# Performance work log

Hardware: AMD Instinct MI355X
Metric: run time of the kernel (lower is better)

## Reference

```python
import jax, jax.numpy as jnp
import numpy as np
from jax import lax


def _conv(x, w):
    # x: [B,H,W,C], w: [kh,kw,Cin,Cout], stride 1, 'same' padding
    return lax.conv_general_dilated(x, w, window_strides=(1, 1), padding='SAME',
                                    dimension_numbers=('NHWC', 'HWIO', 'NHWC'))


def setup_inputs() -> dict:
    key = jax.random.key(0)
    ks = jax.random.split(key, 4)
    B, T, H, W, Cin, F = 16, 5, 256, 256, 3, 8
    return {
        'input_tensor': jax.random.normal(ks[0], (B, T, H, W, Cin), jnp.float32),
        'kernel': jax.random.normal(ks[1], (3, 3, Cin, 4 * F), jnp.float32) * 0.1,
        'recurrent_kernel': jax.random.normal(ks[2], (3, 3, F, 4 * F), jnp.float32) * 0.1,
        'bias': jnp.zeros((4 * F,), jnp.float32),
        'gamma': jnp.ones((F,), jnp.float32),
        'beta': jnp.zeros((F,), jnp.float32),
        'moving_mean': jnp.zeros((F,), jnp.float32),
        'moving_var': jnp.ones((F,), jnp.float32),
        'dense_w': jax.random.normal(ks[3], (F, 2), jnp.float32) * 0.1,
        'dense_b': jnp.zeros((2,), jnp.float32),
    }


def reference(input_tensor, kernel, recurrent_kernel, bias, gamma, beta,
              moving_mean, moving_var, dense_w, dense_b):
    B, T, H, W, Cin = input_tensor.shape
    F = recurrent_kernel.shape[2]
    xs = jnp.moveaxis(input_tensor, 1, 0)  # [T,B,H,W,Cin] time-major for scan
    h0 = jnp.zeros((B, H, W, F), input_tensor.dtype)

    def step(carry, x_t):
        h, c = carry
        # fused 4-gate pre-activations, Keras gate order: i, f, c(g), o
        z = _conv(x_t, kernel) + _conv(h, recurrent_kernel) + bias
        i, f, g, o = jnp.split(z, 4, axis=-1)
        i = jax.nn.sigmoid(i)
        f = jax.nn.sigmoid(f)
        g = jnp.tanh(g)
        o = jax.nn.sigmoid(o)
        c = f * c + i * g
        h = o * jnp.tanh(c)
        return (h, c), None

    (h, _), _ = lax.scan(step, (h0, h0), xs)  # return_sequences=False -> last h

    # BatchNormalization (inference, Keras eps=1e-3)
    eps = 1e-3
    x = (h - moving_mean) * lax.rsqrt(moving_var + eps) * gamma + beta
    # LeakyReLU, Keras default alpha=0.3
    x = jnp.where(x >= 0, x, 0.3 * x)
    # Dense(2) over channel dim
    return jnp.einsum('bhwf,fk->bhwk', x, dense_w) + dense_b
```

## Files before the change

kernel.cpp:

```cpp
#include <hip/hip_runtime.h>


#define BB  16
#define TT  5
#define HH  256
#define WW  256
#define CIN 3
#define FF  8
#define GG  32

#define TW  32
#define THT 16
#define LW  34
#define LH  18
#define NG  8

#define SW  30
#define SH  14
#define NPX 9
#define NPY 19

#define LOG2E 1.44269504088896340736f

typedef _Float16 half8  __attribute__((ext_vector_type(8)));
typedef _Float16 half4  __attribute__((ext_vector_type(4)));
typedef _Float16 half2t __attribute__((ext_vector_type(2)));
typedef float    floatx4 __attribute__((ext_vector_type(4)));

__device__ __forceinline__ float frcp(float x) { return __builtin_amdgcn_rcpf(x); }
__device__ __forceinline__ float sig2(float z)  { return frcp(1.0f + __builtin_amdgcn_exp2f(z)); }
__device__ __forceinline__ float tanh2(float z) { return 1.0f - 2.0f * frcp(1.0f + __builtin_amdgcn_exp2f(z)); }

__device__ __forceinline__ int clampi(int v, int lo, int hi) {
    return v < lo ? lo : (v > hi ? hi : v);
}

#define MFMA(A, B, C) __builtin_amdgcn_mfma_f32_16x16x32_f16((A), (B), (C), 0, 0, 0)

#define GATES(ACC0, ACC1, C0, C1, CN0, CN1, HN0, HN1)                         \
  float CN0, CN1, HN0, HN1;                                                   \
  {                                                                           \
    float s0 = lo8 ? ACC0[2] : ACC0[0]; float r0 = __shfl_xor(s0, 8, 64);     \
    float s1 = lo8 ? ACC0[3] : ACC0[1]; float r1 = __shfl_xor(s1, 8, 64);     \
    float s2 = lo8 ? ACC1[2] : ACC1[0]; float r2 = __shfl_xor(s2, 8, 64);     \
    float s3 = lo8 ? ACC1[3] : ACC1[1]; float r3 = __shfl_xor(s3, 8, 64);     \
    const float zi0 = lo8 ? ACC0[0] : r0, zi1 = lo8 ? ACC0[1] : r1;           \
    const float zf0 = lo8 ? r0 : ACC0[2], zf1 = lo8 ? r1 : ACC0[3];           \
    const float zg0 = lo8 ? ACC1[0] : r2, zg1 = lo8 ? ACC1[1] : r3;           \
    const float zo0 = lo8 ? r2 : ACC1[2], zo1 = lo8 ? r3 : ACC1[3];           \
    const float ii0 = sig2(zi0), ff0 = sig2(zf0), gg0 = tanh2(zg0), oo0 = sig2(zo0); \
    CN0 = ff0 * (C0) + ii0 * gg0;                                             \
    HN0 = oo0 * tanh2(CN0 * (2.0f * LOG2E));                                  \
    const float ii1 = sig2(zi1), ff1 = sig2(zf1), gg1 = tanh2(zg1), oo1 = sig2(zo1); \
    CN1 = ff1 * (C1) + ii1 * gg1;                                             \
    HN1 = oo1 * tanh2(CN1 * (2.0f * LOG2E));                                  \
  }

__global__ void build_frags(const float* __restrict__ wk,
                            const float* __restrict__ wr,
                            _Float16* __restrict__ blob) {
    const int lane = threadIdx.x & 63;
    const int quad = lane >> 4, nlo = lane & 15;
    for (int chunk = 0; chunk < 5; ++chunk) {
        for (int nh = 0; nh < 2; ++nh) {
            const int n = nh * 16 + nlo;
            const float scale = (n >= 16 && n < 24) ? (2.0f * LOG2E) : (-LOG2E);
            const int frag = chunk * 2 + nh;
            _Float16* dhi = blob + ((size_t)frag * 64 + lane) * 8;
            _Float16* dlo = (chunk >= 2)
                ? blob + ((size_t)(10 + (chunk - 2) * 2 + nh) * 64 + lane) * 8
                : nullptr;
            for (int j = 0; j < 8; ++j) {
                const int k = quad * 8 + j;
                float w = 0.0f;
                if (chunk == 0) {
                    int tap = k >> 2, ci = k & 3;
                    if (ci < 3) w = wk[(tap * 3 + ci) * GG + n];
                } else if (chunk == 1) {
                    if (quad == 0 && j < 3) w = wk[(8 * 3 + j) * GG + n];
                } else {
                    int c = chunk - 2;
                    int tap = c * 4 + quad, ci = j;
                    if (tap < 9) w = wr[(tap * FF + ci) * GG + n];
                }
                w *= scale;
                _Float16 wh = (_Float16)w;
                dhi[j] = wh;
                if (dlo) dlo[j] = (_Float16)(w - (float)wh);
            }
        }
    }
}

template <int FIRSTPAIR>
__global__ __launch_bounds__(256) void lstm_pair(
    const float* __restrict__ xg,
    int t,
    const _Float16* __restrict__ blob,
    const float* __restrict__ bias,
    const _Float16* __restrict__ hin,
    _Float16* __restrict__ hout,
    const _Float16* __restrict__ cin,
    _Float16* __restrict__ cout)
{
    __shared__ half8 hls1[LH * LW];
    __shared__ half4 xls1[LH * LW];
    __shared__ half4 xls2[THT * TW];
    __shared__ __align__(16) _Float16 hls2[THT * TW * FF];

    const int tid  = threadIdx.x;
    const int lane = tid & 63, wave = tid >> 6;
    const int quad = lane >> 4, nlo = lane & 15;
    const bool lo8 = (nlo < 8);
    const int fc = nlo & 7;
    const int m0 = quad * 4 + (lo8 ? 0 : 2);

    const int bx = blockIdx.x, by = blockIdx.y, b = blockIdx.z;
    const int x0 = bx * SW - 1, y0 = by * SH - 1;

    half8 bfh[10], bfl[6];
#pragma unroll
    for (int i = 0; i < 10; ++i)
        bfh[i] = *(const half8*)(blob + ((size_t)i * 64 + lane) * 8);
#pragma unroll
    for (int i = 0; i < 6; ++i)
        bfl[i] = *(const half8*)(blob + ((size_t)(10 + i) * 64 + lane) * 8);

    const float bv0 = bias[nlo] * (-LOG2E);
    const float bv1 = bias[16 + nlo] * (lo8 ? 2.0f * LOG2E : -LOG2E);

    float xr1[3][3];
    bool  xin1[3];
#pragma unroll
    for (int k = 0; k < 3; ++k) {
        const int l = tid + k * 256;
        const bool in = (l < LH * LW);
        xin1[k] = in;
        int r = l / LW, c = l - r * LW;
        int gy = y0 - 1 + r, gx = x0 - 1 + c;
        const bool inb = in && (unsigned)gy < HH && (unsigned)gx < WW;
        const float* p = xg + (((size_t)(b * TT + t) * HH + gy) * WW + gx) * CIN;
        xr1[k][0] = inb ? p[0] : 0.0f;
        xr1[k][1] = inb ? p[1] : 0.0f;
        xr1[k][2] = inb ? p[2] : 0.0f;
    }
    float xr2[2][3];
#pragma unroll
    for (int k = 0; k < 2; ++k) {
        const int l = tid + k * 256;
        int r = l >> 5, c = l & 31;
        int gy = y0 + r, gx = x0 + c;
        const bool inb = (unsigned)gy < HH && (unsigned)gx < WW;
        const float* p = xg + (((size_t)(b * TT + t + 1) * HH + gy) * WW + gx) * CIN;
        xr2[k][0] = inb ? p[0] : 0.0f;
        xr2[k][1] = inb ? p[1] : 0.0f;
        xr2[k][2] = inb ? p[2] : 0.0f;
    }
    half8 hr[3];
    if (!FIRSTPAIR) {
#pragma unroll
        for (int k = 0; k < 3; ++k) {
            const int l = tid + k * 256;
            const bool in = (l < LH * LW);
            int r = l / LW, c = l - r * LW;
            int gy = y0 - 1 + r, gx = x0 - 1 + c;
            const bool inb = in && (unsigned)gy < HH && (unsigned)gx < WW;
            half8 v = {(_Float16)0, (_Float16)0, (_Float16)0, (_Float16)0,
                       (_Float16)0, (_Float16)0, (_Float16)0, (_Float16)0};
            if (inb) v = *(const half8*)(hin + ((size_t)(b * HH + gy) * WW + gx) * FF);
            hr[k] = v;
        }
    }
    half2t cpre[NG];
    if (!FIRSTPAIR) {
#pragma unroll
        for (int g = 0; g < NG; ++g) {
            const int lr  = wave * 4 + (g >> 1);
            const int gx0 = (g & 1) * 16;
            const int gy  = y0 + lr;
            const int gxa = x0 + gx0 + m0;
            const bool iny = (unsigned)gy < HH;
            half2t cv; cv.x = (_Float16)0; cv.y = (_Float16)0;
            const _Float16* cp = cin + ((size_t)(b * HH + gy) * WW + gxa) * FF + fc;
            if (iny && (unsigned)gxa < WW)       cv.x = cp[0];
            if (iny && (unsigned)(gxa + 1) < WW) cv.y = cp[FF];
            cpre[g] = cv;
        }
    }

#pragma unroll
    for (int k = 0; k < 3; ++k) {
        if (xin1[k]) {
            half4 vh;
            vh.x = (_Float16)xr1[k][0];
            vh.y = (_Float16)xr1[k][1];
            vh.z = (_Float16)xr1[k][2];
            vh.w = (_Float16)0;
            xls1[tid + k * 256] = vh;
        }
    }
#pragma unroll
    for (int k = 0; k < 2; ++k) {
        half4 vh;
        vh.x = (_Float16)xr2[k][0];
        vh.y = (_Float16)xr2[k][1];
        vh.z = (_Float16)xr2[k][2];
        vh.w = (_Float16)0;
        xls2[tid + k * 256] = vh;
    }
    if (!FIRSTPAIR) {
#pragma unroll
        for (int k = 0; k < 3; ++k)
            if (xin1[k]) hls1[tid + k * 256] = hr[k];
    }
    __syncthreads();

    half2t creg[NG];
#pragma unroll
    for (int g = 0; g < NG; ++g) {
        const int lr  = wave * 4 + (g >> 1);
        const int gx0 = (g & 1) * 16;
        const int lc  = gx0 + nlo;

        const int t0 = 2 * quad, t1 = t0 + 1;
        half4 p  = xls1[(lr + t0 / 3) * LW + lc + t0 % 3];
        half4 q  = xls1[(lr + t1 / 3) * LW + lc + t1 % 3];
        half4 s8 = xls1[(lr + 2) * LW + lc + 2];
        half8 a_xA = (half8){p.x, p.y, p.z, p.w, q.x, q.y, q.z, q.w};
        half8 a_xB = (half8){s8.x, s8.y, s8.z, s8.w, s8.x, s8.y, s8.z, s8.w};

        floatx4 acc0 = {bv0, bv0, bv0, bv0};
        floatx4 acc1 = {bv1, bv1, bv1, bv1};
        acc0 = MFMA(a_xA, bfh[0], acc0);  acc1 = MFMA(a_xA, bfh[1], acc1);
        acc0 = MFMA(a_xB, bfh[2], acc0);  acc1 = MFMA(a_xB, bfh[3], acc1);
        if (!FIRSTPAIR) {
#pragma unroll
            for (int c = 0; c < 3; ++c) {
                int tap = c * 4 + quad;
                if (tap > 8) tap = 8;
                half8 ah = hls1[(lr + tap / 3) * LW + lc + tap % 3];
                acc0 = MFMA(ah, bfh[4 + c * 2], acc0);
                acc1 = MFMA(ah, bfh[5 + c * 2], acc1);
                acc0 = MFMA(ah, bfl[c * 2 + 0], acc0);
                acc1 = MFMA(ah, bfl[c * 2 + 1], acc1);
            }
        }

        const float c0 = FIRSTPAIR ? 0.0f : (float)cpre[g].x;
        const float c1 = FIRSTPAIR ? 0.0f : (float)cpre[g].y;
        GATES(acc0, acc1, c0, c1, cn0, cn1, hn0, hn1);

        half2t cc; cc.x = (_Float16)cn0; cc.y = (_Float16)cn1;
        creg[g] = cc;

        const int gy   = y0 + lr;
        const int colm = gx0 + m0;
        const int gxa  = x0 + colm;
        const bool iny = (unsigned)gy < HH;
        _Float16 h0v = (_Float16)hn0, h1v = (_Float16)hn1;
        if (!(iny && (unsigned)gxa < WW))       h0v = (_Float16)0;
        if (!(iny && (unsigned)(gxa + 1) < WW)) h1v = (_Float16)0;
        hls2[(lr * TW + colm) * FF + fc]     = h0v;
        hls2[(lr * TW + colm + 1) * FF + fc] = h1v;
    }
    __syncthreads();

#pragma unroll
    for (int g = 0; g < NG; ++g) {
        const int lr  = wave * 4 + (g >> 1);
        const int gx0 = (g & 1) * 16;
        const int lc  = gx0 + nlo;

        const int t0 = 2 * quad, t1 = t0 + 1;
        half4 p  = xls2[clampi(lr + t0 / 3 - 1, 0, THT - 1) * TW + clampi(lc + t0 % 3 - 1, 0, TW - 1)];
        half4 q  = xls2[clampi(lr + t1 / 3 - 1, 0, THT - 1) * TW + clampi(lc + t1 % 3 - 1, 0, TW - 1)];
        half4 s8 = xls2[clampi(lr + 1, 0, THT - 1) * TW + clampi(lc + 1, 0, TW - 1)];
        half8 a_xA = (half8){p.x, p.y, p.z, p.w, q.x, q.y, q.z, q.w};
        half8 a_xB = (half8){s8.x, s8.y, s8.z, s8.w, s8.x, s8.y, s8.z, s8.w};

        floatx4 acc0 = {bv0, bv0, bv0, bv0};
        floatx4 acc1 = {bv1, bv1, bv1, bv1};
        acc0 = MFMA(a_xA, bfh[0], acc0);  acc1 = MFMA(a_xA, bfh[1], acc1);
        acc0 = MFMA(a_xB, bfh[2], acc0);  acc1 = MFMA(a_xB, bfh[3], acc1);
#pragma unroll
        for (int c = 0; c < 3; ++c) {
            int tap = c * 4 + quad;
            if (tap > 8) tap = 8;
            const int rr = clampi(lr + tap / 3 - 1, 0, THT - 1);
            const int cc = clampi(lc + tap % 3 - 1, 0, TW - 1);
            half8 ah = *(const half8*)(hls2 + (rr * TW + cc) * FF);
            acc0 = MFMA(ah, bfh[4 + c * 2], acc0);
            acc1 = MFMA(ah, bfh[5 + c * 2], acc1);
            acc0 = MFMA(ah, bfl[c * 2 + 0], acc0);
            acc1 = MFMA(ah, bfl[c * 2 + 1], acc1);
        }

        GATES(acc0, acc1, (float)creg[g].x, (float)creg[g].y, cn0, cn1, hn0, hn1);

        const int gy   = y0 + lr;
        const int colm = gx0 + m0;
        const int gxa  = x0 + colm;
        const bool rowok = (lr >= 1) && (lr <= SH) && ((unsigned)gy < HH);
        const bool c0ok = rowok && (colm >= 1) && (colm <= SW) && ((unsigned)gxa < WW);
        const bool c1ok = rowok && (colm + 1 <= SW) && ((unsigned)(gxa + 1) < WW);
        const size_t base = ((size_t)(b * HH + gy) * WW + gxa) * FF + fc;
        if (c0ok) {
            hout[base] = (_Float16)hn0;
            cout[base] = (_Float16)cn0;
        }
        if (c1ok) {
            hout[base + FF] = (_Float16)hn1;
            cout[base + FF] = (_Float16)cn1;
        }
    }
}

__global__ __launch_bounds__(256) void lstm_last(
    const float* __restrict__ xg,
    const _Float16* __restrict__ blob,
    const float* __restrict__ bias,
    const _Float16* __restrict__ hin,
    const _Float16* __restrict__ cin,
    const float* __restrict__ gamma, const float* __restrict__ beta,
    const float* __restrict__ mean,  const float* __restrict__ var,
    const float* __restrict__ dw,    const float* __restrict__ db,
    float* __restrict__ out)
{
    __shared__ half8 hls[LH * LW];
    __shared__ half4 xls[LH * LW];

    const int tid  = threadIdx.x;
    const int lane = tid & 63, wave = tid >> 6;
    const int quad = lane >> 4, nlo = lane & 15;
    const bool lo8 = (nlo < 8);
    const int fc = nlo & 7;
    const int m0 = quad * 4 + (lo8 ? 0 : 2);
    const int bx = blockIdx.x, by = blockIdx.y, b = blockIdx.z;
    const int t = TT - 1;

    half8 bfh[10], bfl[6];
#pragma unroll
    for (int i = 0; i < 10; ++i)
        bfh[i] = *(const half8*)(blob + ((size_t)i * 64 + lane) * 8);
#pragma unroll
    for (int i = 0; i < 6; ++i)
        bfl[i] = *(const half8*)(blob + ((size_t)(10 + i) * 64 + lane) * 8);

    const float bv0 = bias[nlo] * (-LOG2E);
    const float bv1 = bias[16 + nlo] * (lo8 ? 2.0f * LOG2E : -LOG2E);

    float xr[3][3];
    bool  xin[3];
#pragma unroll
    for (int k = 0; k < 3; ++k) {
        const int l = tid + k * 256;
        const bool in = (l < LH * LW);
        xin[k] = in;
        int r = l / LW, c = l - r * LW;
        int gy = by * THT + r - 1, gx = bx * TW + c - 1;
        const bool inb = in && (unsigned)gy < HH && (unsigned)gx < WW;
        const float* p = xg + (((size_t)(b * TT + t) * HH + gy) * WW + gx) * CIN;
        xr[k][0] = inb ? p[0] : 0.0f;
        xr[k][1] = inb ? p[1] : 0.0f;
        xr[k][2] = inb ? p[2] : 0.0f;
    }
    half8 hr[3];
#pragma unroll
    for (int k = 0; k < 3; ++k) {
        const int l = tid + k * 256;
        const bool in = (l < LH * LW);
        int r = l / LW, c = l - r * LW;
        int gy = by * THT + r - 1, gx = bx * TW + c - 1;
        const bool inb = in && (unsigned)gy < HH && (unsigned)gx < WW;
        half8 v = {(_Float16)0, (_Float16)0, (_Float16)0, (_Float16)0,
                   (_Float16)0, (_Float16)0, (_Float16)0, (_Float16)0};
        if (inb) v = *(const half8*)(hin + ((size_t)(b * HH + gy) * WW + gx) * FF);
        hr[k] = v;
    }
    half2t cpre[NG];
#pragma unroll
    for (int g = 0; g < NG; ++g) {
        const int lr  = wave * 4 + (g >> 1);
        const int gx0 = (g & 1) * 16;
        const int gy  = by * THT + lr;
        const int gxa = bx * TW + gx0 + m0;
        const _Float16* cp = cin + ((size_t)(b * HH + gy) * WW + gxa) * FF + fc;
        half2t cv; cv.x = cp[0]; cv.y = cp[FF];
        cpre[g] = cv;
    }

#pragma unroll
    for (int k = 0; k < 3; ++k) {
        if (xin[k]) {
            half4 vh;
            vh.x = (_Float16)xr[k][0];
            vh.y = (_Float16)xr[k][1];
            vh.z = (_Float16)xr[k][2];
            vh.w = (_Float16)0;
            xls[tid + k * 256] = vh;
            hls[tid + k * 256] = hr[k];
        }
    }
    __syncthreads();

    const float bn_s = gamma[fc] * rsqrtf(var[fc] + 1e-3f);
    const float bn_b = beta[fc] - mean[fc] * bn_s;
    const float dw0 = dw[fc * 2 + 0], dw1 = dw[fc * 2 + 1];
    const float db0 = db[0], db1 = db[1];

#pragma unroll
    for (int g = 0; g < NG; ++g) {
        const int lr  = wave * 4 + (g >> 1);
        const int gx0 = (g & 1) * 16;
        const int lc  = gx0 + nlo;

        const int t0 = 2 * quad, t1 = t0 + 1;
        half4 p  = xls[(lr + t0 / 3) * LW + lc + t0 % 3];
        half4 q  = xls[(lr + t1 / 3) * LW + lc + t1 % 3];
        half4 s8 = xls[(lr + 2) * LW + lc + 2];
        half8 a_xA = (half8){p.x, p.y, p.z, p.w, q.x, q.y, q.z, q.w};
        half8 a_xB = (half8){s8.x, s8.y, s8.z, s8.w, s8.x, s8.y, s8.z, s8.w};

        floatx4 acc0 = {bv0, bv0, bv0, bv0};
        floatx4 acc1 = {bv1, bv1, bv1, bv1};
        acc0 = MFMA(a_xA, bfh[0], acc0);  acc1 = MFMA(a_xA, bfh[1], acc1);
        acc0 = MFMA(a_xB, bfh[2], acc0);  acc1 = MFMA(a_xB, bfh[3], acc1);
#pragma unroll
        for (int c = 0; c < 3; ++c) {
            int tap = c * 4 + quad;
            if (tap > 8) tap = 8;
            half8 ah = hls[(lr + tap / 3) * LW + lc + tap % 3];
            acc0 = MFMA(ah, bfh[4 + c * 2], acc0);
            acc1 = MFMA(ah, bfh[5 + c * 2], acc1);
            acc0 = MFMA(ah, bfl[c * 2 + 0], acc0);
            acc1 = MFMA(ah, bfl[c * 2 + 1], acc1);
        }

        GATES(acc0, acc1, (float)cpre[g].x, (float)cpre[g].y, cn0, cn1, hn0, hn1);
        (void)cn0; (void)cn1;

        const int gy = by * THT + lr;
        float y0 = bn_s * hn0 + bn_b; y0 = (y0 >= 0.f) ? y0 : 0.3f * y0;
        float y1 = bn_s * hn1 + bn_b; y1 = (y1 >= 0.f) ? y1 : 0.3f * y1;
        float p00 = y0 * dw0, p01 = y0 * dw1;
        float p10 = y1 * dw0, p11 = y1 * dw1;
#pragma unroll
        for (int m = 1; m <= 4; m <<= 1) {
            p00 += __shfl_xor(p00, m, 64);
            p01 += __shfl_xor(p01, m, 64);
            p10 += __shfl_xor(p10, m, 64);
            p11 += __shfl_xor(p11, m, 64);
        }
        const int j = nlo & 7;
        if (j < 4) {
            const int px = m0 + (j >> 1);
            const int k  = j & 1;
            float val = (j == 0 ? p00 : j == 1 ? p01 : j == 2 ? p10 : p11)
                        + (k ? db1 : db0);
            out[((size_t)(b * HH + gy) * WW + bx * TW + gx0 + px) * 2 + k] = val;
        }
    }
}

extern "C" void kernel_launch(void* const* d_in, const int* in_sizes, int n_in,
                              void* d_out, int out_size, void* d_ws, size_t ws_size,
                              hipStream_t stream) {
    const float* x     = (const float*)d_in[0];
    const float* wk    = (const float*)d_in[1];
    const float* wr    = (const float*)d_in[2];
    const float* bias  = (const float*)d_in[3];
    const float* gamma = (const float*)d_in[4];
    const float* beta  = (const float*)d_in[5];
    const float* mean  = (const float*)d_in[6];
    const float* var   = (const float*)d_in[7];
    const float* dw    = (const float*)d_in[8];
    const float* db    = (const float*)d_in[9];
    float* out = (float*)d_out;

    const size_t state = (size_t)BB * HH * WW * FF;
    _Float16* blob = (_Float16*)d_ws;
    _Float16* hA = (_Float16*)((char*)d_ws + 32768);
    _Float16* hB = hA + state;
    _Float16* cA = hB + state;
    _Float16* cB = cA + state;

    build_frags<<<1, 64, 0, stream>>>(wk, wr, blob);

    dim3 pgrid(NPX, NPY, BB), block(256);
    lstm_pair<1><<<pgrid, block, 0, stream>>>(x, 0, blob, bias,
                                              nullptr, hA, nullptr, cA);
    lstm_pair<0><<<pgrid, block, 0, stream>>>(x, 2, blob, bias,
                                              hA, hB, cA, cB);
    dim3 lgrid(WW / TW, HH / THT, BB);
    lstm_last<<<lgrid, block, 0, stream>>>(x, blob, bias, hB, cB,
                                           gamma, beta, mean, var, dw, db, out);
}
```

Before: 292.4 us.

## Make lstm_pair persistent with register prefetch of next tile's halo

```diff
diff --git a/kernel.cpp b/kernel.cpp
--- a/kernel.cpp
+++ b/kernel.cpp
@@ -19,6 +19,8 @@
 #define SH  14
 #define NPX 9
 #define NPY 19
+#define NTILE (NPX * NPY * BB)
+#define NBLKP 768
 
 #define LOG2E 1.44269504088896340736f
 
@@ -92,8 +94,37 @@
     }
 }
 
+#define DECODE(TILE, B_, BY_, BX_)                                            \
+    const int B_  = (TILE) / (NPX * NPY);                                     \
+    const int rm_##B_ = (TILE) - B_ * (NPX * NPY);                            \
+    const int BY_ = rm_##B_ / NPX;                                            \
+    const int BX_ = rm_##B_ - BY_ * NPX;
+
+#define PFX1H(TILE, XR, HR, DOH)                                              \
+  {                                                                           \
+    DECODE(TILE, b_, by_, bx_)                                                \
+    const int x0_ = bx_ * SW - 1, y0_ = by_ * SH - 1;                         \
+    _Pragma("unroll")                                                         \
+    for (int k = 0; k < 3; ++k) {                                             \
+      const int l = tid + k * 256;                                            \
+      const int r = l / LW, c = l - r * LW;                                   \
+      const int gy = y0_ - 1 + r, gx = x0_ - 1 + c;                           \
+      const bool inb = xin[k] && (unsigned)gy < HH && (unsigned)gx < WW;      \
+      const float* p = xg + (((size_t)(b_ * TT + t) * HH + gy) * WW + gx) * CIN; \
+      XR[k][0] = inb ? p[0] : 0.0f;                                           \
+      XR[k][1] = inb ? p[1] : 0.0f;                                           \
+      XR[k][2] = inb ? p[2] : 0.0f;                                           \
+      if (DOH) {                                                              \
+        half8 v = {(_Float16)0, (_Float16)0, (_Float16)0, (_Float16)0,        \
+                   (_Float16)0, (_Float16)0, (_Float16)0, (_Float16)0};       \
+        if (inb) v = *(const half8*)(hin + ((size_t)(b_ * HH + gy) * WW + gx) * FF); \
+        HR[k] = v;                                                            \
+      }                                                                       \
+    }                                                                         \
+  }
+
 template <int FIRSTPAIR>
-__global__ __launch_bounds__(256) void lstm_pair(
+__global__ __launch_bounds__(256, 3) void lstm_pair(
     const float* __restrict__ xg,
     int t,
     const _Float16* __restrict__ blob,
@@ -115,8 +146,9 @@
     const int fc = nlo & 7;
     const int m0 = quad * 4 + (lo8 ? 0 : 2);
 
-    const int bx = blockIdx.x, by = blockIdx.y, b = blockIdx.z;
-    const int x0 = bx * SW - 1, y0 = by * SH - 1;
+    bool xin[3];
+#pragma unroll
+    for (int k = 0; k < 3; ++k) xin[k] = (tid + k * 256 < LH * LW);
 
     half8 bfh[10], bfl[6];
 #pragma unroll
@@ -130,187 +162,179 @@
     const float bv1 = bias[16 + nlo] * (lo8 ? 2.0f * LOG2E : -LOG2E);
 
     float xr1[3][3];
-    bool  xin1[3];
-#pragma unroll
-    for (int k = 0; k < 3; ++k) {
-        const int l = tid + k * 256;
-        const bool in = (l < LH * LW);
-        xin1[k] = in;
-        int r = l / LW, c = l - r * LW;
-        int gy = y0 - 1 + r, gx = x0 - 1 + c;
-        const bool inb = in && (unsigned)gy < HH && (unsigned)gx < WW;
-        const float* p = xg + (((size_t)(b * TT + t) * HH + gy) * WW + gx) * CIN;
-        xr1[k][0] = inb ? p[0] : 0.0f;
-        xr1[k][1] = inb ? p[1] : 0.0f;
-        xr1[k][2] = inb ? p[2] : 0.0f;
-    }
-    float xr2[2][3];
-#pragma unroll
-    for (int k = 0; k < 2; ++k) {
-        const int l = tid + k * 256;
-        int r = l >> 5, c = l & 31;
-        int gy = y0 + r, gx = x0 + c;
-        const bool inb = (unsigned)gy < HH && (unsigned)gx < WW;
-        const float* p = xg + (((size_t)(b * TT + t + 1) * HH + gy) * WW + gx) * CIN;
-        xr2[k][0] = inb ? p[0] : 0.0f;
-        xr2[k][1] = inb ? p[1] : 0.0f;
-        xr2[k][2] = inb ? p[2] : 0.0f;
-    }
     half8 hr[3];
-    if (!FIRSTPAIR) {
+    PFX1H((int)blockIdx.x, xr1, hr, !FIRSTPAIR);
+
+#pragma unroll 1
+    for (int tile = (int)blockIdx.x; tile < NTILE; tile += NBLKP) {
+        DECODE(tile, b, by, bx)
+        const int x0 = bx * SW - 1, y0 = by * SH - 1;
+        const int nxt = tile + NBLKP;
+
+        float xr2[2][3];
+#pragma unroll
+        for (int k = 0; k < 2; ++k) {
+            const int l = tid + k * 256;
+            const int r = l >> 5, c = l & 31;
+            const int gy = y0 + r, gx = x0 + c;
+            const bool inb = (unsigned)gy < HH && (unsigned)gx < WW;
+            const float* p = xg + (((size_t)(b * TT + t + 1) * HH + gy) * WW + gx) * CIN;
+            xr2[k][0] = inb ? p[0] : 0.0f;
+            xr2[k][1] = inb ? p[1] : 0.0f;
+            xr2[k][2] = inb ? p[2] : 0.0f;
+        }
+        half2t cpre[NG];
+#pragma unroll
+        for (int g = 0; g < NG; ++g) {
+            half2t cv; cv.x = (_Float16)0; cv.y = (_Float16)0;
+            if (!FIRSTPAIR) {
+                const int lr  = wave * 4 + (g >> 1);
+                const int gx0 = (g & 1) * 16;
+                const int gy  = y0 + lr;
+                const int gxa = x0 + gx0 + m0;
+                const bool iny = (unsigned)gy < HH;
+                const _Float16* cp = cin + ((size_t)(b * HH + gy) * WW + gxa) * FF + fc;
+                if (iny && (unsigned)gxa < WW)       cv.x = cp[0];
+                if (iny && (unsigned)(gxa + 1) < WW) cv.y = cp[FF];
+            }
+            cpre[g] = cv;
+        }
+
+        __syncthreads();
+
 #pragma unroll
         for (int k = 0; k < 3; ++k) {
-            const int l = tid + k * 256;
-            const bool in = (l < LH * LW);
-            int r = l / LW, c = l - r * LW;
-            int gy = y0 - 1 + r, gx = x0 - 1 + c;
-            const bool inb = in && (unsigned)gy < HH && (unsigned)gx < WW;
-            half8 v = {(_Float16)0, (_Float16)0, (_Float16)0, (_Float16)0,
-                       (_Float16)0, (_Float16)0, (_Float16)0, (_Float16)0};
-            if (inb) v = *(const half8*)(hin + ((size_t)(b * HH + gy) * WW + gx) * FF);
-            hr[k] = v;
-        }
-    }
-    half2t cpre[NG];
-    if (!FIRSTPAIR) {
+            if (xin[k]) {
+                half4 vh;
+                vh.x = (_Float16)xr1[k][0];
+                vh.y = (_Float16)xr1[k][1];
+                vh.z = (_Float16)xr1[k][2];
+                vh.w = (_Float16)0;
+                xls1[tid + k * 256] = vh;
+                if (!FIRSTPAIR) hls1[tid + k * 256] = hr[k];
+            }
+        }
+#pragma unroll
+        for (int k = 0; k < 2; ++k) {
+            half4 vh;
+            vh.x = (_Float16)xr2[k][0];
+            vh.y = (_Float16)xr2[k][1];
+            vh.z = (_Float16)xr2[k][2];
+            vh.w = (_Float16)0;
+            xls2[tid + k * 256] = vh;
+        }
+
+        float xr1n[3][3];
+        half8 hrn[3];
+        if (nxt < NTILE) PFX1H(nxt, xr1n, hrn, !FIRSTPAIR);
+
+        __syncthreads();
+
+        half2t creg[NG];
 #pragma unroll
         for (int g = 0; g < NG; ++g) {
             const int lr  = wave * 4 + (g >> 1);
             const int gx0 = (g & 1) * 16;
-            const int gy  = y0 + lr;
-            const int gxa = x0 + gx0 + m0;
+            const int lc  = gx0 + nlo;
+
+            const int t0 = 2 * quad, t1 = t0 + 1;
+            half4 p  = xls1[(lr + t0 / 3) * LW + lc + t0 % 3];
+            half4 q  = xls1[(lr + t1 / 3) * LW + lc + t1 % 3];
+            half4 s8 = xls1[(lr + 2) * LW + lc + 2];
+            half8 a_xA = (half8){p.x, p.y, p.z, p.w, q.x, q.y, q.z, q.w};
+            half8 a_xB = (half8){s8.x, s8.y, s8.z, s8.w, s8.x, s8.y, s8.z, s8.w};
+
+            floatx4 acc0 = {bv0, bv0, bv0, bv0};
+            floatx4 acc1 = {bv1, bv1, bv1, bv1};
+            acc0 = MFMA(a_xA, bfh[0], acc0);  acc1 = MFMA(a_xA, bfh[1], acc1);
+            acc0 = MFMA(a_xB, bfh[2], acc0);  acc1 = MFMA(a_xB, bfh[3], acc1);
+            if (!FIRSTPAIR) {
+#pragma unroll
+                for (int c = 0; c < 3; ++c) {
+                    int tap = c * 4 + quad;
+                    if (tap > 8) tap = 8;
+                    half8 ah = hls1[(lr + tap / 3) * LW + lc + tap % 3];
+                    acc0 = MFMA(ah, bfh[4 + c * 2], acc0);
+                    acc1 = MFMA(ah, bfh[5 + c * 2], acc1);
+                    acc0 = MFMA(ah, bfl[c * 2 + 0], acc0);
+                    acc1 = MFMA(ah, bfl[c * 2 + 1], acc1);
+                }
+            }
+
+            GATES(acc0, acc1, (float)cpre[g].x, (float)cpre[g].y, cn0, cn1, hn0, hn1);
+
+            half2t cc; cc.x = (_Float16)cn0; cc.y = (_Float16)cn1;
+            creg[g] = cc;
+
+            const int gy   = y0 + lr;
+            const int colm = gx0 + m0;
+            const int gxa  = x0 + colm;
             const bool iny = (unsigned)gy < HH;
-            half2t cv; cv.x = (_Float16)0; cv.y = (_Float16)0;
-            const _Float16* cp = cin + ((size_t)(b * HH + gy) * WW + gxa) * FF + fc;
-            if (iny && (unsigned)gxa < WW)       cv.x = cp[0];
-            if (iny && (unsigned)(gxa + 1) < WW) cv.y = cp[FF];
-            cpre[g] = cv;
-        }
-    }
-
-#pragma unroll
-    for (int k = 0; k < 3; ++k) {
-        if (xin1[k]) {
-            half4 vh;
-            vh.x = (_Float16)xr1[k][0];
-            vh.y = (_Float16)xr1[k][1];
-            vh.z = (_Float16)xr1[k][2];
-            vh.w = (_Float16)0;
-            xls1[tid + k * 256] = vh;
-        }
-    }
-#pragma unroll
-    for (int k = 0; k < 2; ++k) {
-        half4 vh;
-        vh.x = (_Float16)xr2[k][0];
-        vh.y = (_Float16)xr2[k][1];
-        vh.z = (_Float16)xr2[k][2];
-        vh.w = (_Float16)0;
-        xls2[tid + k * 256] = vh;
-    }
-    if (!FIRSTPAIR) {
-#pragma unroll
-        for (int k = 0; k < 3; ++k)
-            if (xin1[k]) hls1[tid + k * 256] = hr[k];
-    }
-    __syncthreads();
-
-    half2t creg[NG];
-#pragma unroll
-    for (int g = 0; g < NG; ++g) {
-        const int lr  = wave * 4 + (g >> 1);
-        const int gx0 = (g & 1) * 16;
-        const int lc  = gx0 + nlo;
-
-        const int t0 = 2 * quad, t1 = t0 + 1;
-        half4 p  = xls1[(lr + t0 / 3) * LW + lc + t0 % 3];
-        half4 q  = xls1[(lr + t1 / 3) * LW + lc + t1 % 3];
-        half4 s8 = xls1[(lr + 2) * LW + lc + 2];
-        half8 a_xA = (half8){p.x, p.y, p.z, p.w, q.x, q.y, q.z, q.w};
-        half8 a_xB = (half8){s8.x, s8.y, s8.z, s8.w, s8.x, s8.y, s8.z, s8.w};
-
-        floatx4 acc0 = {bv0, bv0, bv0, bv0};
-        floatx4 acc1 = {bv1, bv1, bv1, bv1};
-        acc0 = MFMA(a_xA, bfh[0], acc0);  acc1 = MFMA(a_xA, bfh[1], acc1);
-        acc0 = MFMA(a_xB, bfh[2], acc0);  acc1 = MFMA(a_xB, bfh[3], acc1);
-        if (!FIRSTPAIR) {
+            _Float16 h0v = (_Float16)hn0, h1v = (_Float16)hn1;
+            if (!(iny && (unsigned)gxa < WW))       h0v = (_Float16)0;
+            if (!(iny && (unsigned)(gxa + 1) < WW)) h1v = (_Float16)0;
+            hls2[(lr * TW + colm) * FF + fc]     = h0v;
+            hls2[(lr * TW + colm + 1) * FF + fc] = h1v;
+        }
+        __syncthreads();
+
+#pragma unroll
+        for (int g = 0; g < NG; ++g) {
+            const int lr  = wave * 4 + (g >> 1);
+            const int gx0 = (g & 1) * 16;
+            const int lc  = gx0 + nlo;
+
+            const int t0 = 2 * quad, t1 = t0 + 1;
+            half4 p  = xls2[clampi(lr + t0 / 3 - 1, 0, THT - 1) * TW + clampi(lc + t0 % 3 - 1, 0, TW - 1)];
+            half4 q  = xls2[clampi(lr + t1 / 3 - 1, 0, THT - 1) * TW + clampi(lc + t1 % 3 - 1, 0, TW - 1)];
+            half4 s8 = xls2[clampi(lr + 1, 0, THT - 1) * TW + clampi(lc + 1, 0, TW - 1)];
+            half8 a_xA = (half8){p.x, p.y, p.z, p.w, q.x, q.y, q.z, q.w};
+            half8 a_xB = (half8){s8.x, s8.y, s8.z, s8.w, s8.x, s8.y, s8.z, s8.w};
+
+            floatx4 acc0 = {bv0, bv0, bv0, bv0};
+            floatx4 acc1 = {bv1, bv1, bv1, bv1};
+            acc0 = MFMA(a_xA, bfh[0], acc0);  acc1 = MFMA(a_xA, bfh[1], acc1);
+            acc0 = MFMA(a_xB, bfh[2], acc0);  acc1 = MFMA(a_xB, bfh[3], acc1);
 #pragma unroll
             for (int c = 0; c < 3; ++c) {
                 int tap = c * 4 + quad;
                 if (tap > 8) tap = 8;
-                half8 ah = hls1[(lr + tap / 3) * LW + lc + tap % 3];
+                const int rr = clampi(lr + tap / 3 - 1, 0, THT - 1);
+                const int cc = clampi(lc + tap % 3 - 1, 0, TW - 1);
+                half8 ah = *(const half8*)(hls2 + (rr * TW + cc) * FF);
                 acc0 = MFMA(ah, bfh[4 + c * 2], acc0);
                 acc1 = MFMA(ah, bfh[5 + c * 2], acc1);
                 acc0 = MFMA(ah, bfl[c * 2 + 0], acc0);
                 acc1 = MFMA(ah, bfl[c * 2 + 1], acc1);
             }
-        }
-
-        const float c0 = FIRSTPAIR ? 0.0f : (float)cpre[g].x;
-        const float c1 = FIRSTPAIR ? 0.0f : (float)cpre[g].y;
-        GATES(acc0, acc1, c0, c1, cn0, cn1, hn0, hn1);
-
-        half2t cc; cc.x = (_Float16)cn0; cc.y = (_Float16)cn1;
-        creg[g] = cc;
-
-        const int gy   = y0 + lr;
-        const int colm = gx0 + m0;
-        const int gxa  = x0 + colm;
-        const bool iny = (unsigned)gy < HH;
-        _Float16 h0v = (_Float16)hn0, h1v = (_Float16)hn1;
-        if (!(iny && (unsigned)gxa < WW))       h0v = (_Float16)0;
-        if (!(iny && (unsigned)(gxa + 1) < WW)) h1v = (_Float16)0;
-        hls2[(lr * TW + colm) * FF + fc]     = h0v;
-        hls2[(lr * TW + colm + 1) * FF + fc] = h1v;
-    }
-    __syncthreads();
-
-#pragma unroll
-    for (int g = 0; g < NG; ++g) {
-        const int lr  = wave * 4 + (g >> 1);
-        const int gx0 = (g & 1) * 16;
-        const int lc  = gx0 + nlo;
-
-        const int t0 = 2 * quad, t1 = t0 + 1;
-        half4 p  = xls2[clampi(lr + t0 / 3 - 1, 0, THT - 1) * TW + clampi(lc + t0 % 3 - 1, 0, TW - 1)];
-        half4 q  = xls2[clampi(lr + t1 / 3 - 1, 0, THT - 1) * TW + clampi(lc + t1 % 3 - 1, 0, TW - 1)];
-        half4 s8 = xls2[clampi(lr + 1, 0, THT - 1) * TW + clampi(lc + 1, 0, TW - 1)];
-        half8 a_xA = (half8){p.x, p.y, p.z, p.w, q.x, q.y, q.z, q.w};
-        half8 a_xB = (half8){s8.x, s8.y, s8.z, s8.w, s8.x, s8.y, s8.z, s8.w};
-
-        floatx4 acc0 = {bv0, bv0, bv0, bv0};
-        floatx4 acc1 = {bv1, bv1, bv1, bv1};
-        acc0 = MFMA(a_xA, bfh[0], acc0);  acc1 = MFMA(a_xA, bfh[1], acc1);
-        acc0 = MFMA(a_xB, bfh[2], acc0);  acc1 = MFMA(a_xB, bfh[3], acc1);
-#pragma unroll
-        for (int c = 0; c < 3; ++c) {
-            int tap = c * 4 + quad;
-            if (tap > 8) tap = 8;
-            const int rr = clampi(lr + tap / 3 - 1, 0, THT - 1);
-            const int cc = clampi(lc + tap % 3 - 1, 0, TW - 1);
-            half8 ah = *(const half8*)(hls2 + (rr * TW + cc) * FF);
-            acc0 = MFMA(ah, bfh[4 + c * 2], acc0);
-            acc1 = MFMA(ah, bfh[5 + c * 2], acc1);
-            acc0 = MFMA(ah, bfl[c * 2 + 0], acc0);
-            acc1 = MFMA(ah, bfl[c * 2 + 1], acc1);
-        }
-
-        GATES(acc0, acc1, (float)creg[g].x, (float)creg[g].y, cn0, cn1, hn0, hn1);
-
-        const int gy   = y0 + lr;
-        const int colm = gx0 + m0;
-        const int gxa  = x0 + colm;
-        const bool rowok = (lr >= 1) && (lr <= SH) && ((unsigned)gy < HH);
-        const bool c0ok = rowok && (colm >= 1) && (colm <= SW) && ((unsigned)gxa < WW);
-        const bool c1ok = rowok && (colm + 1 <= SW) && ((unsigned)(gxa + 1) < WW);
-        const size_t base = ((size_t)(b * HH + gy) * WW + gxa) * FF + fc;
-        if (c0ok) {
-            hout[base] = (_Float16)hn0;
-            cout[base] = (_Float16)cn0;
-        }
-        if (c1ok) {
-            hout[base + FF] = (_Float16)hn1;
-            cout[base + FF] = (_Float16)cn1;
+
+            GATES(acc0, acc1, (float)creg[g].x, (float)creg[g].y, cn0, cn1, hn0, hn1);
+
+            const int gy   = y0 + lr;
+            const int colm = gx0 + m0;
+            const int gxa  = x0 + colm;
+            const bool rowok = (lr >= 1) && (lr <= SH) && ((unsigned)gy < HH);
+            const bool c0ok = rowok && (colm >= 1) && (colm <= SW) && ((unsigned)gxa < WW);
+            const bool c1ok = rowok && (colm + 1 <= SW) && ((unsigned)(gxa + 1) < WW);
+            const size_t base = ((size_t)(b * HH + gy) * WW + gxa) * FF + fc;
+            if (c0ok) {
+                hout[base] = (_Float16)hn0;
+                cout[base] = (_Float16)cn0;
+            }
+            if (c1ok) {
+                hout[base + FF] = (_Float16)hn1;
+                cout[base + FF] = (_Float16)cn1;
+            }
+        }
+
+        if (nxt < NTILE) {
+#pragma unroll
+            for (int k = 0; k < 3; ++k) {
+                xr1[k][0] = xr1n[k][0];
+                xr1[k][1] = xr1n[k][1];
+                xr1[k][2] = xr1n[k][2];
+                if (!FIRSTPAIR) hr[k] = hrn[k];
+            }
         }
     }
 }
@@ -486,11 +510,11 @@
 
     build_frags<<<1, 64, 0, stream>>>(wk, wr, blob);
 
-    dim3 pgrid(NPX, NPY, BB), block(256);
-    lstm_pair<1><<<pgrid, block, 0, stream>>>(x, 0, blob, bias,
-                                              nullptr, hA, nullptr, cA);
-    lstm_pair<0><<<pgrid, block, 0, stream>>>(x, 2, blob, bias,
-                                              hA, hB, cA, cB);
+    dim3 block(256);
+    lstm_pair<1><<<dim3(NBLKP), block, 0, stream>>>(x, 0, blob, bias,
+                                                    nullptr, hA, nullptr, cA);
+    lstm_pair<0><<<dim3(NBLKP), block, 0, stream>>>(x, 2, blob, bias,
+                                                    hA, hB, cA, cB);
     dim3 lgrid(WW / TW, HH / THT, BB);
     lstm_last<<<lgrid, block, 0, stream>>>(x, blob, bias, hB, cB,
                                            gamma, beta, mean, var, dw, db, out);
```

Result: slower. 371.1 us (+26.9%).
